# Optimization experiments

Hardware: AMD Instinct MI355X
Metric: run time of the kernel (lower is better)

The kernel has to match this reference:

```python
import jax, jax.numpy as jnp
import numpy as np

N = 100_000          # nodes
E = 3_200_000        # edges (avg degree 32)
H = 20               # hidden_channels (node feature width, = 10 one-hot + 10 mlp)
EH = 64              # edge_hidden_dim
EO = 10              # edge_output_dim
THRESHOLD = 1.0


def setup_inputs() -> dict:
    key = jax.random.key(0)
    ks = jax.random.split(key, 12)
    x = jax.random.normal(ks[0], (N, 2, H), dtype=jnp.float32)
    edge_index = jax.random.randint(ks[1], (2, E), 0, N, dtype=jnp.int32)
    # distances strictly in (0, threshold]
    edge_attr = jax.random.uniform(ks[2], (E, 1), jnp.float32, 1e-4, THRESHOLD)
    # parameters (torch.rand init as in the module)
    a = jax.random.uniform(ks[3], (1,), jnp.float32)
    b = jax.random.uniform(ks[4], (1,), jnp.float32) + 1.0
    gamma1 = jax.random.uniform(ks[5], (H, H), jnp.float32)
    gamma2 = jax.random.uniform(ks[6], (H, H), jnp.float32)
    bias = jax.random.uniform(ks[7], (H,), jnp.float32)
    # edge MLP: Linear(1, EH) -> ReLU -> Linear(EH, EO)
    W1 = jax.random.normal(ks[8], (1, EH), jnp.float32)
    b1 = jnp.zeros((EH,), jnp.float32)
    W2 = jax.random.normal(ks[9], (EH, EO), jnp.float32) / np.sqrt(EH)
    b2 = jnp.zeros((EO,), jnp.float32)
    return dict(x=x, edge_index=edge_index, edge_attr=edge_attr, a=a, b=b,
                gamma1=gamma1, gamma2=gamma2, bias=bias, W1=W1, b1=b1, W2=W2, b2=b2)


def reference(x, edge_index, edge_attr, a, b, gamma1, gamma2, bias, W1, b1, W2, b2):
    src, dst = edge_index[0], edge_index[1]
    # --- edge features ---
    h = jax.nn.relu(edge_attr @ W1 + b1)            # [E, EH]
    mlp_out = h @ W2 + b2                           # [E, EO]
    # one-hot distance bucket: 10 equal intervals over (0, threshold], idx 10 -> 9
    idx = jnp.clip((edge_attr[:, 0] * (10.0 / THRESHOLD)).astype(jnp.int32), 0, 9)
    one_hot = jax.nn.one_hot(idx, 10, dtype=x.dtype)  # [E, 10]
    eac = jnp.concatenate([one_hot, mlp_out], axis=1)  # edge_attr_combined [E, 20]
    # --- per-source-node normalization (w_tilde) ---
    sum_w = jax.ops.segment_sum(eac, src, num_segments=N)  # [N, 20]
    sw = sum_w[src]                                        # [E, 20]
    safe = jnp.where(sw != 0, sw, 1.0)
    w_tilde = jnp.where(sw != 0, eac / safe, jnp.asarray(0.01, x.dtype))
    # --- rho weighting on node features ---
    h_j = x[src, 0]                                  # [E, 20]
    h_jp = x[dst, 0]                                 # [E, 20]
    rho = jnp.abs(a * h_j - (1.0 - a) * h_jp) ** b   # [E, 20]
    # --- aggregate messages per source node ---
    sum_features = jax.ops.segment_sum(rho * w_tilde, src, num_segments=N)  # [N, 20]
    # --- node update ---
    out0 = jax.nn.sigmoid(x[:, 0] @ gamma1.T + sum_features @ gamma2.T + bias)
    return jnp.stack([out0, sum_features], axis=1)   # [N, 2, 20]
```

## Files before the change

kernel.cpp:

```cpp
#include <hip/hip_runtime.h>
#include <hip/hip_bf16.h>


#define BATCH 4096
#define BPT   16
#define BSH   7
#define CAP   4608

__device__ int block_scan_excl(int* data, int n, int* scratch) {
    const int t = threadIdx.x;
    const int lane = t & 63, w = t >> 6;
    const int base = t * 4;
    int v0 = (base + 0 < n) ? data[base + 0] : 0;
    int v1 = (base + 1 < n) ? data[base + 1] : 0;
    int v2 = (base + 2 < n) ? data[base + 2] : 0;
    int v3 = (base + 3 < n) ? data[base + 3] : 0;
    int p1 = v0 + v1, p2 = p1 + v2, p3 = p2 + v3;
    int x = p3;
    #pragma unroll
    for (int o = 1; o < 64; o <<= 1) { int y = __shfl_up(x, o); if (lane >= o) x += y; }
    if (lane == 63) scratch[w] = x;
    __syncthreads();
    int wbase = 0;
    for (int i = 0; i < w; ++i) wbase += scratch[i];
    int tb = wbase + x - p3;
    if (base + 0 < n) data[base + 0] = tb;
    if (base + 1 < n) data[base + 1] = tb + v0;
    if (base + 2 < n) data[base + 2] = tb + p1;
    if (base + 3 < n) data[base + 3] = tb + p2;
    int tot = scratch[0] + scratch[1] + scratch[2] + scratch[3];
    __syncthreads();
    return tot;
}

__launch_bounds__(256)
__global__ void k_bcount(const int* __restrict__ src, int* __restrict__ bcount,
                         const float* __restrict__ x, __hip_bfloat16* __restrict__ xa,
                         int E, int nb, int N) {
    __shared__ int lc[1024];
    const int t = threadIdx.x;
    for (int i = t; i < 1024; i += 256) lc[i] = 0;
    __syncthreads();
    const int base = blockIdx.x * BATCH;
    #pragma unroll
    for (int k = 0; k < BPT; ++k) {
        int e = base + k * 256 + t;
        if (e < E) atomicAdd(&lc[src[e] >> BSH], 1);
    }
    __syncthreads();
    for (int i = t; i < nb; i += 256) { int c = lc[i]; if (c) atomicAdd(&bcount[i], c); }
    const int stride = gridDim.x * 256;
    for (int i = blockIdx.x * 256 + t; i < N * 20; i += stride) {
        int n = i / 20, c = i - n * 20;
        xa[(n << 5) + c] = __float2bfloat16(x[n * 40 + c]);
    }
}

__global__ void k_bscan(int* __restrict__ bcount, int* __restrict__ bstart,
                        int* __restrict__ gcursor, int nb,
                        const float* __restrict__ W1, const float* __restrict__ b1,
                        const float* __restrict__ W2, const float* __restrict__ b2,
                        float* __restrict__ AB, int* __restrict__ flag,
                        int EH, int EO) {
    __shared__ int scratch[4];
    int total = block_scan_excl(bcount, nb, scratch);
    const int t = threadIdx.x;
    for (int i = t; i < nb; i += 256) { bstart[i] = bcount[i]; gcursor[i] = bcount[i]; }
    if (t == 0) bstart[nb] = total;
    if (t == 64) {
        int ok = 1;
        for (int k = 0; k < EH; ++k) if (b1[k] != 0.0f) ok = 0;
        *flag = ok;
    }
    if (t < EO) {
        float A = 0.0f;
        for (int k = 0; k < EH; ++k)
            if (W1[k] > 0.0f) A = fmaf(W1[k], W2[k * EO + t], A);
        AB[t]      = A;
        AB[EO + t] = b2[t];
    }
}

__launch_bounds__(256)
__global__ void k_bscatter(const int* __restrict__ src, const int* __restrict__ dst,
                           const float* __restrict__ ea, int* __restrict__ gcursor,
                           int2* __restrict__ tmp, int E, int nb) {
    __shared__ int  pay[BATCH];
    __shared__ unsigned char pbn[BATCH];
    __shared__ unsigned short sbid[BATCH];
    __shared__ int  lcount[1024];
    __shared__ int  lsave[1024];
    __shared__ int  scratch[4];
    const int t = threadIdx.x;
    for (int i = t; i < 1024; i += 256) lcount[i] = 0;
    __syncthreads();
    const int base = blockIdx.x * BATCH;
    int mys[BPT], myr[BPT], myw[BPT];
    #pragma unroll
    for (int k = 0; k < BPT; ++k) {
        int e = base + k * 256 + t;
        mys[k] = -1;
        if (e < E) {
            int s = src[e], d = dst[e];
            float dd = ea[e];
            int ib = (int)(dd * 10.0f);
            ib = ib < 0 ? 0 : (ib > 9 ? 9 : ib);
            int dq = (int)fmaf(dd, 2047.0f, 0.5f);
            dq = dq < 0 ? 0 : (dq > 2047 ? 2047 : dq);
            mys[k] = s;
            myr[k] = atomicAdd(&lcount[s >> BSH], 1);
            myw[k] = (d & 0x1FFFF) | (ib << 17) | (dq << 21);
        }
    }
    __syncthreads();
    for (int i = t; i < 1024; i += 256) lsave[i] = lcount[i];
    __syncthreads();
    int total = block_scan_excl(lcount, nb, scratch);
    for (int b = t; b < nb; b += 256) {
        int c = lsave[b];
        if (c > 0) lsave[b] = atomicAdd(&gcursor[b], c);
    }
    __syncthreads();
    #pragma unroll
    for (int k = 0; k < BPT; ++k) {
        if (mys[k] >= 0) {
            int b = mys[k] >> BSH;
            int pos = lcount[b] + myr[k];
            pay[pos]  = myw[k];
            pbn[pos]  = (unsigned char)(mys[k] & 127);
            sbid[pos] = (unsigned short)b;
        }
    }
    __syncthreads();
    for (int j = t; j < total; j += 256) {
        int b = sbid[j];
        tmp[lsave[b] + (j - lcount[b])] = make_int2(pay[j], (int)pbn[j]);
    }
}

template <int USE_XA>
__launch_bounds__(512, 8)
__global__ void k_nodeb(const float* __restrict__ x,
                        const __hip_bfloat16* __restrict__ xa,
                        const int* __restrict__ bstart,
                        const int2* __restrict__ tmp,
                        const float* __restrict__ a_p, const float* __restrict__ b_p,
                        const float* __restrict__ g1, const float* __restrict__ g2,
                        const float* __restrict__ bias,
                        const float* __restrict__ AB, const int* __restrict__ flag_p,
                        const float* __restrict__ W1, const float* __restrict__ b1,
                        const float* __restrict__ W2, const float* __restrict__ b2,
                        float* __restrict__ out, int N, int EH, int EO) {
    __shared__ int   buf[CAP];
    __shared__ int   hist[128];
    __shared__ int   rowstart[129];
    __shared__ int   lcur[128];
    __shared__ unsigned char perm[128];
    __shared__ __hip_bfloat16 s_x0[128 * 22];
    __shared__ float s_sf[128 * 21];
    __shared__ float s_g1[20 * 21], s_g2[20 * 21], s_b[20];

    const int t = threadIdx.x;
    const int b = blockIdx.x;
    const int node0 = b << BSH;
    const int s0 = bstart[b];
    const int m  = bstart[b + 1] - s0;

    if (t < 128) hist[t] = 0;
    for (int i = t; i < 400; i += 512) {
        int r = i / 20, cc = i - r * 20;
        s_g1[r * 21 + cc] = g1[i];
        s_g2[r * 21 + cc] = g2[i];
    }
    if (t < 20) s_b[t] = bias[t];
    for (int i = t; i < 2560; i += 512) {
        int l = i / 20, cc = i - l * 20;
        int n = node0 + l;
        s_x0[l * 22 + cc] = __float2bfloat16((n < N) ? x[n * 40 + cc] : 0.0f);
    }
    __syncthreads();

    int vw[9], vn[9];
    #pragma unroll
    for (int k = 0; k < 9; ++k) {
        int i = k * 512 + t;
        vn[k] = -1;
        if (i < m && i < CAP) {
            int2 v = tmp[s0 + i];
            vw[k] = v.x;
            vn[k] = v.y & 127;
            atomicAdd(&hist[vn[k]], 1);
        }
    }
    __syncthreads();
    if (t < 64) {
        int a = hist[2 * t], bb = hist[2 * t + 1];
        int s = a + bb;
        int xsc = s;
        #pragma unroll
        for (int o = 1; o < 64; o <<= 1) { int y = __shfl_up(xsc, o); if (t >= o) xsc += y; }
        int excl = xsc - s;
        rowstart[2 * t]     = excl;
        rowstart[2 * t + 1] = excl + a;
        lcur[2 * t]         = excl;
        lcur[2 * t + 1]     = excl + a;
        if (t == 63) rowstart[128] = xsc;
    }
    __syncthreads();
    #pragma unroll
    for (int k = 0; k < 9; ++k) {
        if (vn[k] >= 0) {
            int p = atomicAdd(&lcur[vn[k]], 1);
            if (p < CAP) buf[p] = vw[k];
        }
    }
    __syncthreads();

    if (t < 128) hist[t] = 0;
    __syncthreads();
    if (t < 128) {
        int len = rowstart[t + 1] - rowstart[t];
        int bin = 127 - (len > 127 ? 127 : len);
        atomicAdd(&hist[bin], 1);
    }
    __syncthreads();
    if (t < 64) {
        int a = hist[2 * t], bb = hist[2 * t + 1];
        int s = a + bb;
        int xsc = s;
        #pragma unroll
        for (int o = 1; o < 64; o <<= 1) { int y = __shfl_up(xsc, o); if (t >= o) xsc += y; }
        int excl = xsc - s;
        hist[2 * t]     = excl;
        hist[2 * t + 1] = excl + a;
    }
    __syncthreads();
    if (t < 128) {
        int len = rowstart[t + 1] - rowstart[t];
        int bin = 127 - (len > 127 ? 127 : len);
        int pos = atomicAdd(&hist[bin], 1);
        perm[pos] = (unsigned char)t;
    }

    const float av = a_p[0], bv = b_p[0];
    const float am1 = 1.0f - av;
    const int fl = *flag_p;
    __syncthreads();

    #pragma unroll
    for (int r = 0; r < 5; ++r) {
        int item = t + 512 * r;
        int li = perm[item / 20];
        int c = item - (item / 20) * 20;
        const bool cl10 = c < 10;
        float x0c = __bfloat162float(s_x0[li * 22 + c]);
        const float pax = av * x0c;
        int rs = rowstart[li];
        int re = rowstart[li + 1];
        float sf;
        if (fl || cl10) {
            float sA = 0.0f, sB = 0.0f, s2 = 0.0f;
            int i = rs;
            for (; i + 4 <= re; i += 4) {
                int w0 = buf[i + 0];
                int w1 = buf[i + 1];
                int w2 = buf[i + 2];
                int w3 = buf[i + 3];
                float xd0, xd1, xd2, xd3;
                if (USE_XA) {
                    xd0 = __bfloat162float(xa[((w0 & 0x1FFFF) << 5) + c]);
                    xd1 = __bfloat162float(xa[((w1 & 0x1FFFF) << 5) + c]);
                    xd2 = __bfloat162float(xa[((w2 & 0x1FFFF) << 5) + c]);
                    xd3 = __bfloat162float(xa[((w3 & 0x1FFFF) << 5) + c]);
                } else {
                    xd0 = x[(w0 & 0x1FFFF) * 40 + c];
                    xd1 = x[(w1 & 0x1FFFF) * 40 + c];
                    xd2 = x[(w2 & 0x1FFFF) * 40 + c];
                    xd3 = x[(w3 & 0x1FFFF) * 40 + c];
                }
                #define STEP(w_, xd_)                                          \
                {                                                              \
                    float tt_  = fabsf(fmaf(-am1, (xd_), pax));                \
                    float rho_ = exp2f(bv * __log2f(tt_));                     \
                    int   ib_  = ((w_) >> 17) & 0xF;                           \
                    float dqf_ = (float)(((unsigned)(w_)) >> 21);              \
                    float sel_ = cl10 ? ((ib_ == c) ? 1.0f : 0.0f) : dqf_;     \
                    sA += sel_;                                                \
                    sB = fmaf(rho_, sel_, sB);                                 \
                    s2 += rho_;                                                \
                }
                STEP(w0, xd0); STEP(w1, xd1); STEP(w2, xd2); STEP(w3, xd3);
            }
            for (; i < re; ++i) {
                int w0 = buf[i];
                float xd0 = USE_XA ? __bfloat162float(xa[((w0 & 0x1FFFF) << 5) + c])
                                   : x[(w0 & 0x1FFFF) * 40 + c];
                STEP(w0, xd0);
            }
            float sw, s1;
            if (cl10) { sw = sA; s1 = sB; }
            else {
                float Afq = AB[c - 10] * (1.0f / 2047.0f);
                float Bf  = AB[c];
                float deg = (float)(re - rs);
                sw = fmaf(Afq, sA, Bf * deg);
                s1 = fmaf(Afq, sB, Bf * s2);
            }
            sf = (sw != 0.0f) ? (s1 / sw) : (0.01f * s2);
        } else {
            float sw = 0.0f, s1 = 0.0f, s2 = 0.0f;
            for (int i = rs; i < re; ++i) {
                int w0 = buf[i];
                float xd0 = USE_XA ? __bfloat162float(xa[((w0 & 0x1FFFF) << 5) + c])
                                   : x[(w0 & 0x1FFFF) * 40 + c];
                float dd_ = (float)(((unsigned)w0) >> 21) * (1.0f / 2047.0f);
                float m_ = b2[c - 10];
                for (int k_ = 0; k_ < EH; ++k_) {
                    float h_ = fmaf(dd_, W1[k_], b1[k_]);
                    h_ = h_ > 0.0f ? h_ : 0.0f;
                    m_ = fmaf(h_, W2[k_ * EO + (c - 10)], m_);
                }
                float tt_  = fabsf(fmaf(-am1, xd0, pax));
                float rho_ = exp2f(bv * __log2f(tt_));
                sw += m_;
                s1 = fmaf(rho_, m_, s1);
                s2 += rho_;
            }
            sf = (sw != 0.0f) ? (s1 / sw) : (0.01f * s2);
        }
        s_sf[li * 21 + c] = sf;
    }
    __syncthreads();

    for (int i = t; i < 2560; i += 512) {
        int l = i / 20, cc = i - l * 20;
        int n = node0 + l;
        if (n < N) {
            float acc = s_b[cc];
            const __hip_bfloat16* xr = &s_x0[l * 22];
            const float* sr  = &s_sf[l * 21];
            const float* g1r = &s_g1[cc * 21];
            const float* g2r = &s_g2[cc * 21];
            #pragma unroll
            for (int k = 0; k < 20; ++k)
                acc = fmaf(__bfloat162float(xr[k]), g1r[k], fmaf(sr[k], g2r[k], acc));
            float o0 = 1.0f / (1.0f + __expf(-acc));
            out[n * 40 + cc]      = o0;
            out[n * 40 + 20 + cc] = sr[cc];
        }
    }
}

extern "C" void kernel_launch(void* const* d_in, const int* in_sizes, int n_in,
                              void* d_out, int out_size, void* d_ws, size_t ws_size,
                              hipStream_t stream) {
    const float* x    = (const float*)d_in[0];
    const int*   ei   = (const int*)  d_in[1];
    const float* ea   = (const float*)d_in[2];
    const float* a_p  = (const float*)d_in[3];
    const float* b_p  = (const float*)d_in[4];
    const float* g1   = (const float*)d_in[5];
    const float* g2   = (const float*)d_in[6];
    const float* bias = (const float*)d_in[7];
    const float* W1   = (const float*)d_in[8];
    const float* b1   = (const float*)d_in[9];
    const float* W2   = (const float*)d_in[10];
    const float* b2   = (const float*)d_in[11];
    float* out = (float*)d_out;

    const int E  = in_sizes[2];
    const int N  = in_sizes[0] / 40;
    const int EH = in_sizes[8];
    const int EO = in_sizes[11];
    const int* src = ei;
    const int* dst = ei + E;

    const int nb     = (N + 127) >> BSH;
    const int nbatch = (E + BATCH - 1) / BATCH;

    int* ws_i = (int*)d_ws;
    size_t o = 0;
    int* bcount  = ws_i + o; o += (size_t)nb;       o = (o + 1) & ~(size_t)1;
    int* bstart  = ws_i + o; o += (size_t)(nb + 1); o = (o + 1) & ~(size_t)1;
    int* gcursor = ws_i + o; o += (size_t)nb;       o = (o + 1) & ~(size_t)1;
    float* AB    = (float*)(ws_i + o); o += 2 * (size_t)EO;
    int* flag    = ws_i + o; o += 1;                o = (o + 1) & ~(size_t)1;
    int2* tmp    = (int2*)(ws_i + o); o += 2 * (size_t)E;
    __hip_bfloat16* xa = (__hip_bfloat16*)(ws_i + o);
    const size_t need_xa = o * 4 + (size_t)N * 32 * 2;
    const int use_xa = (ws_size >= need_xa) ? 1 : 0;

    hipMemsetAsync(bcount, 0, (size_t)nb * sizeof(int), stream);

    k_bcount  <<<nbatch, 256, 0, stream>>>(src, bcount, x, use_xa ? xa : (__hip_bfloat16*)AB,
                                           E, nb, use_xa ? N : 0);
    k_bscan   <<<1,      256, 0, stream>>>(bcount, bstart, gcursor, nb,
                                           W1, b1, W2, b2, AB, flag, EH, EO);
    k_bscatter<<<nbatch, 256, 0, stream>>>(src, dst, ea, gcursor, tmp, E, nb);
    if (use_xa) {
        k_nodeb<1><<<nb, 512, 0, stream>>>(x, xa, bstart, tmp, a_p, b_p,
                                           g1, g2, bias, AB, flag,
                                           W1, b1, W2, b2, out, N, EH, EO);
    } else {
        k_nodeb<0><<<nb, 512, 0, stream>>>(x, xa, bstart, tmp, a_p, b_p,
                                           g1, g2, bias, AB, flag,
                                           W1, b1, W2, b2, out, N, EH, EO);
    }
}
```

Baseline: 264.7 us.

## Replace count+scan+scatter with fixed-capacity bucket scatter and split SoA payload

Drops the counting pass and single-block scan by giving each 128-node bucket a fixed CAP-sized slot, so one scatter kernel writes edges directly using atomic cursors. The edge payload is split into an int word array and a byte node-index array, and the node kernel reads them vectorised. The bf16 x repack, the parameter precompute and a software-pipelined gather loop are folded in. It saves two launches and a full pass over src, but edges past CAP per bucket are silently dropped. The repacked xa written by k_scatter is now read by k_nodeb to fill s_x0.

```diff
diff --git a/kernel.cpp b/kernel.cpp
--- a/kernel.cpp
+++ b/kernel.cpp
@@ -34,57 +34,14 @@
 }
 
 __launch_bounds__(256)
-__global__ void k_bcount(const int* __restrict__ src, int* __restrict__ bcount,
-                         const float* __restrict__ x, __hip_bfloat16* __restrict__ xa,
-                         int E, int nb, int N) {
-    __shared__ int lc[1024];
-    const int t = threadIdx.x;
-    for (int i = t; i < 1024; i += 256) lc[i] = 0;
-    __syncthreads();
-    const int base = blockIdx.x * BATCH;
-    #pragma unroll
-    for (int k = 0; k < BPT; ++k) {
-        int e = base + k * 256 + t;
-        if (e < E) atomicAdd(&lc[src[e] >> BSH], 1);
-    }
-    __syncthreads();
-    for (int i = t; i < nb; i += 256) { int c = lc[i]; if (c) atomicAdd(&bcount[i], c); }
-    const int stride = gridDim.x * 256;
-    for (int i = blockIdx.x * 256 + t; i < N * 20; i += stride) {
-        int n = i / 20, c = i - n * 20;
-        xa[(n << 5) + c] = __float2bfloat16(x[n * 40 + c]);
-    }
-}
-
-__global__ void k_bscan(int* __restrict__ bcount, int* __restrict__ bstart,
-                        int* __restrict__ gcursor, int nb,
-                        const float* __restrict__ W1, const float* __restrict__ b1,
-                        const float* __restrict__ W2, const float* __restrict__ b2,
-                        float* __restrict__ AB, int* __restrict__ flag,
-                        int EH, int EO) {
-    __shared__ int scratch[4];
-    int total = block_scan_excl(bcount, nb, scratch);
-    const int t = threadIdx.x;
-    for (int i = t; i < nb; i += 256) { bstart[i] = bcount[i]; gcursor[i] = bcount[i]; }
-    if (t == 0) bstart[nb] = total;
-    if (t == 64) {
-        int ok = 1;
-        for (int k = 0; k < EH; ++k) if (b1[k] != 0.0f) ok = 0;
-        *flag = ok;
-    }
-    if (t < EO) {
-        float A = 0.0f;
-        for (int k = 0; k < EH; ++k)
-            if (W1[k] > 0.0f) A = fmaf(W1[k], W2[k * EO + t], A);
-        AB[t]      = A;
-        AB[EO + t] = b2[t];
-    }
-}
-
-__launch_bounds__(256)
-__global__ void k_bscatter(const int* __restrict__ src, const int* __restrict__ dst,
-                           const float* __restrict__ ea, int* __restrict__ gcursor,
-                           int2* __restrict__ tmp, int E, int nb) {
+__global__ void k_scatter(const int* __restrict__ src, const int* __restrict__ dst,
+                          const float* __restrict__ ea, int* __restrict__ gcursor,
+                          int* __restrict__ tmpw, unsigned char* __restrict__ tmpn,
+                          const float* __restrict__ x, __hip_bfloat16* __restrict__ xa,
+                          const float* __restrict__ W1, const float* __restrict__ b1,
+                          const float* __restrict__ W2, const float* __restrict__ b2,
+                          float* __restrict__ AB, int* __restrict__ flag,
+                          int E, int nb, int Npack, int EH, int EO) {
     __shared__ int  pay[BATCH];
     __shared__ unsigned char pbn[BATCH];
     __shared__ unsigned short sbid[BATCH];
@@ -92,6 +49,22 @@
     __shared__ int  lsave[1024];
     __shared__ int  scratch[4];
     const int t = threadIdx.x;
+
+    if (blockIdx.x == 0) {
+        if (t == 64) {
+            int ok = 1;
+            for (int k = 0; k < EH; ++k) if (b1[k] != 0.0f) ok = 0;
+            *flag = ok;
+        }
+        if (t < EO) {
+            float A = 0.0f;
+            for (int k = 0; k < EH; ++k)
+                if (W1[k] > 0.0f) A = fmaf(W1[k], W2[k * EO + t], A);
+            AB[t]      = A;
+            AB[EO + t] = b2[t];
+        }
+    }
+
     for (int i = t; i < 1024; i += 256) lcount[i] = 0;
     __syncthreads();
     const int base = blockIdx.x * BATCH;
@@ -134,7 +107,16 @@
     __syncthreads();
     for (int j = t; j < total; j += 256) {
         int b = sbid[j];
-        tmp[lsave[b] + (j - lcount[b])] = make_int2(pay[j], (int)pbn[j]);
+        int pos = lsave[b] + (j - lcount[b]);
+        if (pos < CAP) {
+            tmpw[b * CAP + pos] = pay[j];
+            tmpn[b * CAP + pos] = pbn[j];
+        }
+    }
+    const int stride = gridDim.x * 256;
+    for (int i = blockIdx.x * 256 + t; i < Npack * 20; i += stride) {
+        int n = i / 20, c = i - n * 20;
+        xa[(n << 5) + c] = __float2bfloat16(x[n * 40 + c]);
     }
 }
 
@@ -142,8 +124,9 @@
 __launch_bounds__(512, 8)
 __global__ void k_nodeb(const float* __restrict__ x,
                         const __hip_bfloat16* __restrict__ xa,
-                        const int* __restrict__ bstart,
-                        const int2* __restrict__ tmp,
+                        const int* __restrict__ gcount,
+                        const int* __restrict__ tmpw,
+                        const unsigned char* __restrict__ tmpn,
                         const float* __restrict__ a_p, const float* __restrict__ b_p,
                         const float* __restrict__ g1, const float* __restrict__ g2,
                         const float* __restrict__ bias,
@@ -163,8 +146,9 @@
     const int t = threadIdx.x;
     const int b = blockIdx.x;
     const int node0 = b << BSH;
-    const int s0 = bstart[b];
-    const int m  = bstart[b + 1] - s0;
+    const int s0 = b * CAP;
+    int m = gcount[b];
+    if (m > CAP) m = CAP;
 
     if (t < 128) hist[t] = 0;
     for (int i = t; i < 400; i += 512) {
@@ -176,20 +160,31 @@
     for (int i = t; i < 2560; i += 512) {
         int l = i / 20, cc = i - l * 20;
         int n = node0 + l;
-        s_x0[l * 22 + cc] = __float2bfloat16((n < N) ? x[n * 40 + cc] : 0.0f);
-    }
-    __syncthreads();
-
-    int vw[9], vn[9];
-    #pragma unroll
-    for (int k = 0; k < 9; ++k) {
-        int i = k * 512 + t;
-        vn[k] = -1;
-        if (i < m && i < CAP) {
-            int2 v = tmp[s0 + i];
-            vw[k] = v.x;
-            vn[k] = v.y & 127;
-            atomicAdd(&hist[vn[k]], 1);
+        if (USE_XA)
+            s_x0[l * 22 + cc] = (n < N) ? xa[(n << 5) + cc] : __float2bfloat16(0.0f);
+        else
+            s_x0[l * 22 + cc] = __float2bfloat16((n < N) ? x[n * 40 + cc] : 0.0f);
+    }
+    __syncthreads();
+
+    const int4*   tw4 = (const int4*)(tmpw + s0);
+    const uchar4* tn4 = (const uchar4*)(tmpn + s0);
+    int vw[12], vn[12];
+    #pragma unroll
+    for (int k = 0; k < 3; ++k) {
+        int idx4 = k * 512 + t;
+        #pragma unroll
+        for (int j = 0; j < 4; ++j) vn[k * 4 + j] = -1;
+        int e0 = idx4 << 2;
+        if (e0 < m) {
+            int4   wv = tw4[idx4];
+            uchar4 nv = tn4[idx4];
+            vw[k * 4 + 0] = wv.x; vw[k * 4 + 1] = wv.y;
+            vw[k * 4 + 2] = wv.z; vw[k * 4 + 3] = wv.w;
+            { vn[k * 4 + 0] = nv.x & 127; atomicAdd(&hist[vn[k * 4 + 0]], 1); }
+            if (e0 + 1 < m) { vn[k * 4 + 1] = nv.y & 127; atomicAdd(&hist[vn[k * 4 + 1]], 1); }
+            if (e0 + 2 < m) { vn[k * 4 + 2] = nv.z & 127; atomicAdd(&hist[vn[k * 4 + 2]], 1); }
+            if (e0 + 3 < m) { vn[k * 4 + 3] = nv.w & 127; atomicAdd(&hist[vn[k * 4 + 3]], 1); }
         }
     }
     __syncthreads();
@@ -208,10 +203,10 @@
     }
     __syncthreads();
     #pragma unroll
-    for (int k = 0; k < 9; ++k) {
+    for (int k = 0; k < 12; ++k) {
         if (vn[k] >= 0) {
             int p = atomicAdd(&lcur[vn[k]], 1);
-            if (p < CAP) buf[p] = vw[k];
+            buf[p] = vw[k];
         }
     }
     __syncthreads();
@@ -246,6 +241,20 @@
     const float am1 = 1.0f - av;
     const int fl = *flag_p;
     __syncthreads();
+
+#define GATH(w_) (USE_XA ? __bfloat162float(xa[(((w_) & 0x1FFFF) << 5) + c]) \
+                         : x[((w_) & 0x1FFFF) * 40 + c])
+#define STEP(w_, xd_)                                          \
+{                                                              \
+    float tt_  = fabsf(fmaf(-am1, (xd_), pax));                \
+    float rho_ = exp2f(bv * __log2f(tt_));                     \
+    int   ib_  = ((w_) >> 17) & 0xF;                           \
+    float dqf_ = (float)(((unsigned)(w_)) >> 21);              \
+    float sel_ = cl10 ? ((ib_ == c) ? 1.0f : 0.0f) : dqf_;     \
+    sA += sel_;                                                \
+    sB = fmaf(rho_, sel_, sB);                                 \
+    s2 += rho_;                                                \
+}
 
     #pragma unroll
     for (int r = 0; r < 5; ++r) {
@@ -261,40 +270,21 @@
         if (fl || cl10) {
             float sA = 0.0f, sB = 0.0f, s2 = 0.0f;
             int i = rs;
-            for (; i + 4 <= re; i += 4) {
-                int w0 = buf[i + 0];
-                int w1 = buf[i + 1];
-                int w2 = buf[i + 2];
-                int w3 = buf[i + 3];
-                float xd0, xd1, xd2, xd3;
-                if (USE_XA) {
-                    xd0 = __bfloat162float(xa[((w0 & 0x1FFFF) << 5) + c]);
-                    xd1 = __bfloat162float(xa[((w1 & 0x1FFFF) << 5) + c]);
-                    xd2 = __bfloat162float(xa[((w2 & 0x1FFFF) << 5) + c]);
-                    xd3 = __bfloat162float(xa[((w3 & 0x1FFFF) << 5) + c]);
-                } else {
-                    xd0 = x[(w0 & 0x1FFFF) * 40 + c];
-                    xd1 = x[(w1 & 0x1FFFF) * 40 + c];
-                    xd2 = x[(w2 & 0x1FFFF) * 40 + c];
-                    xd3 = x[(w3 & 0x1FFFF) * 40 + c];
-                }
-                #define STEP(w_, xd_)                                          \
-                {                                                              \
-                    float tt_  = fabsf(fmaf(-am1, (xd_), pax));                \
-                    float rho_ = exp2f(bv * __log2f(tt_));                     \
-                    int   ib_  = ((w_) >> 17) & 0xF;                           \
-                    float dqf_ = (float)(((unsigned)(w_)) >> 21);              \
-                    float sel_ = cl10 ? ((ib_ == c) ? 1.0f : 0.0f) : dqf_;     \
-                    sA += sel_;                                                \
-                    sB = fmaf(rho_, sel_, sB);                                 \
-                    s2 += rho_;                                                \
+            if (i + 4 <= re) {
+                int w0 = buf[i + 0], w1 = buf[i + 1], w2 = buf[i + 2], w3 = buf[i + 3];
+                float xd0 = GATH(w0), xd1 = GATH(w1), xd2 = GATH(w2), xd3 = GATH(w3);
+                for (i += 4; i + 4 <= re; i += 4) {
+                    int u0 = buf[i + 0], u1 = buf[i + 1], u2 = buf[i + 2], u3 = buf[i + 3];
+                    float yd0 = GATH(u0), yd1 = GATH(u1), yd2 = GATH(u2), yd3 = GATH(u3);
+                    STEP(w0, xd0); STEP(w1, xd1); STEP(w2, xd2); STEP(w3, xd3);
+                    w0 = u0; w1 = u1; w2 = u2; w3 = u3;
+                    xd0 = yd0; xd1 = yd1; xd2 = yd2; xd3 = yd3;
                 }
                 STEP(w0, xd0); STEP(w1, xd1); STEP(w2, xd2); STEP(w3, xd3);
             }
             for (; i < re; ++i) {
                 int w0 = buf[i];
-                float xd0 = USE_XA ? __bfloat162float(xa[((w0 & 0x1FFFF) << 5) + c])
-                                   : x[(w0 & 0x1FFFF) * 40 + c];
+                float xd0 = GATH(w0);
                 STEP(w0, xd0);
             }
             float sw, s1;
@@ -311,8 +301,7 @@
             float sw = 0.0f, s1 = 0.0f, s2 = 0.0f;
             for (int i = rs; i < re; ++i) {
                 int w0 = buf[i];
-                float xd0 = USE_XA ? __bfloat162float(xa[((w0 & 0x1FFFF) << 5) + c])
-                                   : x[(w0 & 0x1FFFF) * 40 + c];
+                float xd0 = GATH(w0);
                 float dd_ = (float)(((unsigned)w0) >> 21) * (1.0f / 2047.0f);
                 float m_ = b2[c - 10];
                 for (int k_ = 0; k_ < EH; ++k_) {
@@ -378,31 +367,30 @@
     const int nb     = (N + 127) >> BSH;
     const int nbatch = (E + BATCH - 1) / BATCH;
 
-    int* ws_i = (int*)d_ws;
+    char* wsb = (char*)d_ws;
     size_t o = 0;
-    int* bcount  = ws_i + o; o += (size_t)nb;       o = (o + 1) & ~(size_t)1;
-    int* bstart  = ws_i + o; o += (size_t)(nb + 1); o = (o + 1) & ~(size_t)1;
-    int* gcursor = ws_i + o; o += (size_t)nb;       o = (o + 1) & ~(size_t)1;
-    float* AB    = (float*)(ws_i + o); o += 2 * (size_t)EO;
-    int* flag    = ws_i + o; o += 1;                o = (o + 1) & ~(size_t)1;
-    int2* tmp    = (int2*)(ws_i + o); o += 2 * (size_t)E;
-    __hip_bfloat16* xa = (__hip_bfloat16*)(ws_i + o);
-    const size_t need_xa = o * 4 + (size_t)N * 32 * 2;
+    int* gcursor = (int*)(wsb + o); o += (size_t)nb * 4;        o = (o + 15) & ~(size_t)15;
+    float* AB    = (float*)(wsb + o); o += 2 * (size_t)EO * 4;
+    int* flag    = (int*)(wsb + o);   o += 4;                   o = (o + 15) & ~(size_t)15;
+    int* tmpw    = (int*)(wsb + o);   o += (size_t)nb * CAP * 4;
+    unsigned char* tmpn = (unsigned char*)(wsb + o); o += (size_t)nb * CAP;
+    o = (o + 15) & ~(size_t)15;
+    __hip_bfloat16* xa = (__hip_bfloat16*)(wsb + o);
+    const size_t need_xa = o + (size_t)N * 32 * 2;
     const int use_xa = (ws_size >= need_xa) ? 1 : 0;
 
-    hipMemsetAsync(bcount, 0, (size_t)nb * sizeof(int), stream);
-
-    k_bcount  <<<nbatch, 256, 0, stream>>>(src, bcount, x, use_xa ? xa : (__hip_bfloat16*)AB,
-                                           E, nb, use_xa ? N : 0);
-    k_bscan   <<<1,      256, 0, stream>>>(bcount, bstart, gcursor, nb,
-                                           W1, b1, W2, b2, AB, flag, EH, EO);
-    k_bscatter<<<nbatch, 256, 0, stream>>>(src, dst, ea, gcursor, tmp, E, nb);
+    hipMemsetAsync(gcursor, 0, (size_t)nb * sizeof(int), stream);
+
+    k_scatter<<<nbatch, 256, 0, stream>>>(src, dst, ea, gcursor, tmpw, tmpn,
+                                          x, use_xa ? xa : (__hip_bfloat16*)AB,
+                                          W1, b1, W2, b2, AB, flag,
+                                          E, nb, use_xa ? N : 0, EH, EO);
     if (use_xa) {
-        k_nodeb<1><<<nb, 512, 0, stream>>>(x, xa, bstart, tmp, a_p, b_p,
+        k_nodeb<1><<<nb, 512, 0, stream>>>(x, xa, gcursor, tmpw, tmpn, a_p, b_p,
                                            g1, g2, bias, AB, flag,
                                            W1, b1, W2, b2, out, N, EH, EO);
     } else {
-        k_nodeb<0><<<nb, 512, 0, stream>>>(x, xa, bstart, tmp, a_p, b_p,
+        k_nodeb<0><<<nb, 512, 0, stream>>>(x, xa, gcursor, tmpw, tmpn, a_p, b_p,
                                            g1, g2, bias, AB, flag,
                                            W1, b1, W2, b2, out, N, EH, EO);
     }
```

Measured after the change: 243.9 us. 7.8% less time.
